# Optimization experiments

Hardware: AMD Instinct MI355X
Metric: run time of the kernel (lower is better)

The kernel has to match this reference:

```python
import jax, jax.numpy as jnp
import numpy as np

B, IC, OC, K, H, W = 8, 512, 512, 3, 32, 32
GAIN, LRMUL = 1.0, 1.0
# compute_runtime_coef: fan_in = prod(weight_shape[:-1])
RC_CONV = GAIN / np.sqrt(K * K * IC) * LRMUL   # conv weight [K,K,IC,OC]
RC_DENSE = GAIN / np.sqrt(IC) * LRMUL          # dense weight [IC, IC]


def setup_inputs() -> dict:
    key = jax.random.key(0)
    ks = jax.random.split(key, 4)
    x = jax.random.normal(ks[0], (B, IC, H, W), dtype=jnp.float32)
    w = jax.random.normal(ks[1], (B, IC), dtype=jnp.float32)
    # init_std = 1/lrmul = 1.0 for both weights; bias init zeros
    conv_w = jax.random.normal(ks[2], (K, K, IC, OC), dtype=jnp.float32)
    dense_w = jax.random.normal(ks[3], (IC, IC), dtype=jnp.float32)
    dense_b = jnp.zeros((IC,), dtype=jnp.float32)
    return {"x": x, "w": w, "conv_w": conv_w, "dense_w": dense_w, "dense_b": dense_b}


def reference(x, w, conv_w, dense_w, dense_b):
    b, ic, h, wd = x.shape
    # modulation: style = Dense(w) + bias + 1
    style = w @ (RC_DENSE * dense_w) + LRMUL * dense_b + 1.0        # [B, IC]
    wt = (RC_CONV * conv_w)[None] * style[:, None, None, :, None]   # [B,K,K,IC,OC]
    # demodulation: rsqrt of sum of squares over (kh, kw, ic)
    d = jax.lax.rsqrt(jnp.sum(jnp.square(wt), axis=(1, 2, 3)) + 1e-8)  # [B, OC]
    wt = wt * d[:, None, None, None, :]
    # grouped conv with groups = batch: weight -> OIHW [B*OC, IC, K, K]
    w_g = jnp.transpose(wt, (0, 4, 3, 1, 2)).reshape(b * OC, ic, K, K)
    xg = x.reshape(1, b * ic, h, wd)
    y = jax.lax.conv_general_dilated(
        xg, w_g, window_strides=(1, 1), padding="SAME",
        dimension_numbers=("NCHW", "OIHW", "NCHW"), feature_group_count=b)
    return y.reshape(b, OC, h, wd)
```

## Files before the change

### kernel.cpp

```cpp
#include <hip/hip_runtime.h>
#include <stdint.h>


#define B_   8
#define IC_  512
#define OC_  512

static constexpr float RC_DENSE = 0.04419417382415922f;
static constexpr float RC_CONV  = 0.014731391274719739f;

typedef _Float16 half8    __attribute__((ext_vector_type(8)));
typedef float    floatx16 __attribute__((ext_vector_type(16)));

__device__ __forceinline__ void g2l(const void* g, void* l) {
  __builtin_amdgcn_global_load_lds(
      (const __attribute__((address_space(1))) void*)g,
      (__attribute__((address_space(3))) void*)l, 16, 0, 0);
}

__global__ __launch_bounds__(256) void style_kernel(
    const float* __restrict__ wv, const float* __restrict__ dw,
    const float* __restrict__ db, float* __restrict__ sm,
    float* __restrict__ sm2) {
  const int b = blockIdx.y;
  const int i = blockIdx.x * 64 + (threadIdx.x & 63);
  const int jg = threadIdx.x >> 6;
  __shared__ float red[4][64];
  float p = 0.f;
  for (int j = jg * 128; j < jg * 128 + 128; ++j)
    p += wv[b * IC_ + j] * dw[(size_t)j * IC_ + i];
  red[jg][threadIdx.x & 63] = p;
  __syncthreads();
  if (threadIdx.x < 64) {
    float s = red[0][threadIdx.x] + red[1][threadIdx.x] +
              red[2][threadIdx.x] + red[3][threadIdx.x];
    s = s * RC_DENSE + db[i] + 1.0f;
    float v = s * RC_CONV;
    sm[b * IC_ + i] = v;
    sm2[b * IC_ + i] = v * v;
  }
}

__global__ __launch_bounds__(256) void prep_kernel(
    const float* __restrict__ cw, const float* __restrict__ x,
    const float* __restrict__ sm, const float* __restrict__ sm2,
    _Float16* __restrict__ Wtf, float* __restrict__ dpart,
    _Float16* __restrict__ xsp) {
  __shared__ __align__(16) char smem[33280];
  const int bid = blockIdx.x;
  const int tid = threadIdx.x;
  if (bid < 256) {
    _Float16* LA = (_Float16*)smem;
    float* redall = (float*)(smem + 18432);
    const int by2 = bid >> 4, icb = bid & 15;
    const int by = by2 >> 1, h2 = by2 & 1;
    const int oc0 = by * 64 + h2 * 32, ic0 = icb * 32;
    const int ocl = tid & 31, g = tid >> 5;
    float sq4[4] = {};
    for (int m = 0; m < 36; ++m) {
      int r = m * 8 + g;
      int t = r >> 5, icl = r & 31;
      float v = cw[(size_t)(t * IC_ + ic0 + icl) * OC_ + oc0 + ocl];
      sq4[m & 3] += v * v;
      LA[m * 256 + ocl * 8 + g] = (_Float16)v;
    }
    for (int b = 0; b < 8; ++b) {
      float p = 0.f;
      for (int s = 0; s < 4; ++s)
        p += sm2[b * IC_ + ic0 + g + 8 * s] * sq4[s];
      redall[(b * 8 + g) * 32 + ocl] = p;
    }
    __syncthreads();
    _Float16* dst = Wtf + (size_t)(by * 16 + icb) * 18432;
    for (int it = 0; it < 5; ++it) {
      int c = it * 256 + tid;
      if (c < 1152) {
        int m = c >> 5, o2 = c & 31;
        *(half8*)(dst + (size_t)(m * 64 + h2 * 32 + o2) * 8) =
            *(const half8*)&LA[m * 256 + o2 * 8];
      }
    }
    const int bb = tid >> 5, o3 = tid & 31;
    float s = 0.f;
    for (int g2 = 0; g2 < 8; ++g2) s += redall[(bb * 8 + g2) * 32 + o3];
    dpart[(size_t)icb * 4096 + bb * OC_ + oc0 + o3] = s;
  } else {
    _Float16* Xt = (_Float16*)smem;
    const int rb = bid - 256;
    const int b = rb >> 5, h = rb & 31;
    for (int k = 0; k < 16; ++k) {
      int idx = k * 256 + tid;
      int ic = idx >> 3, wc = (idx & 7) * 4;
      float4 v = *(const float4*)&x[((size_t)(b * IC_ + ic) * 32 + h) * 32 + wc];
      float s = sm[b * IC_ + ic];
      Xt[(wc + 0) * 520 + ic] = (_Float16)(v.x * s);
      Xt[(wc + 1) * 520 + ic] = (_Float16)(v.y * s);
      Xt[(wc + 2) * 520 + ic] = (_Float16)(v.z * s);
      Xt[(wc + 3) * 520 + ic] = (_Float16)(v.w * s);
    }
    __syncthreads();
    _Float16* xb = xsp + (size_t)b * 16 * 36992;
    const int r = h + 1;
    half8 z = {};
    for (int it = 0; it < 9; ++it) {
      int c = it * 256 + tid;
      if (c < 2176) {
        int icb = c / 136, rem = c - 136 * icb, kkq = rem / 34, C = rem - 34 * kkq;
        half8 val = z;
        if (C != 0 && C != 33)
          val = *(const half8*)&Xt[(C - 1) * 520 + icb * 32 + kkq * 8];
        *(half8*)&xb[(size_t)icb * 36992 + (size_t)r * 1088 + kkq * 272 + C * 8] = val;
      }
    }
    if (h == 0 || h == 31) {
      const int rz = (h == 0) ? 0 : 33;
      for (int it = 0; it < 9; ++it) {
        int c = it * 256 + tid;
        if (c < 2176) {
          int icb = c / 136, rem = c - 136 * icb, kkq = rem / 34, C = rem - 34 * kkq;
          *(half8*)&xb[(size_t)icb * 36992 + (size_t)rz * 1088 + kkq * 272 + C * 8] = z;
        }
      }
    }
  }
}

__global__ __launch_bounds__(256) void conv_kernel(
    const _Float16* __restrict__ Wtf,
    const _Float16* __restrict__ xsp,
    const float* __restrict__ dpart,
    float* __restrict__ out) {
  const int by = blockIdx.x, bx = blockIdx.y, b = blockIdx.z;
  const int tid = threadIdx.x, lane = tid & 63, w = tid >> 6;
  const int wm = w & 1, wn = w >> 1;
  const int n = lane & 31, kq = lane >> 5;
  const int h0 = bx * 4;

  __shared__ _Float16 Xb[2][6528];
  __shared__ float redd[4][64];
  __shared__ float dvl[64];

  const _Float16* gX = xsp + (size_t)b * 16 * 36992 + (size_t)h0 * 1088;
  const _Float16* gA = Wtf + (size_t)(by * 16) * 18432;
  const int aoff = kq * 512 + (wm * 32 + n) * 8;

  for (int i = 0; i < 4; ++i) {
    int c = i * 256 + tid;
    if (c < 816) g2l(gX + (size_t)c * 8, &Xb[0][c * 8]);
  }
  half8 a[9][2], an[9][2];
#pragma unroll
  for (int t = 0; t < 9; ++t)
#pragma unroll
    for (int kk = 0; kk < 2; ++kk)
      a[t][kk] = *(const half8*)(gA + aoff + (t * 2 + kk) * 1024);

  floatx16 acc[2] = {};
  for (int icb = 0; icb < 16; ++icb) {
    const int cur = icb & 1;
    __syncthreads();
    if (icb < 15) {
      const _Float16* gA1 = gA + (size_t)(icb + 1) * 18432 + aoff;
#pragma unroll
      for (int t = 0; t < 9; ++t)
#pragma unroll
        for (int kk = 0; kk < 2; ++kk)
          an[t][kk] = *(const half8*)(gA1 + (t * 2 + kk) * 1024);
      const _Float16* gX1 = gX + (size_t)(icb + 1) * 36992;
      for (int i = 0; i < 4; ++i) {
        int c = i * 256 + tid;
        if (c < 816) g2l(gX1 + (size_t)c * 8, &Xb[cur ^ 1][c * 8]);
      }
    }
    const _Float16* Xp = &Xb[cur][0] + (wn * 2) * 1088 + kq * 272 + n * 8;
#pragma unroll
    for (int s = 0; s < 4; ++s) {
#pragma unroll
      for (int kw = 0; kw < 3; ++kw) {
#pragma unroll
        for (int kk = 0; kk < 2; ++kk) {
          half8 xv = *(const half8*)(Xp + s * 1088 + kk * 544 + kw * 8);
#pragma unroll
          for (int kh = 0; kh < 3; ++kh) {
            int j = s - kh;
            if (j >= 0 && j < 2)
              acc[j] = __builtin_amdgcn_mfma_f32_32x32x16_f16(
                  a[kh * 3 + kw][kk], xv, acc[j], 0, 0, 0);
          }
        }
      }
    }
#pragma unroll
    for (int t = 0; t < 9; ++t) { a[t][0] = an[t][0]; a[t][1] = an[t][1]; }
  }

  __syncthreads();
  {
    const int oc_l = tid & 63, ig = tid >> 6;
    float s = 0.f;
    for (int k = 0; k < 4; ++k)
      s += dpart[(size_t)(ig * 4 + k) * 4096 + b * OC_ + by * 64 + oc_l];
    redd[ig][oc_l] = s;
  }
  __syncthreads();
  if (tid < 64)
    dvl[tid] = rsqrtf(redd[0][tid] + redd[1][tid] + redd[2][tid] +
                      redd[3][tid] + 1e-8f);
  __syncthreads();
  const int oc0 = by * 64 + wm * 32;
  const int r0 = h0 + wn * 2;
#pragma unroll
  for (int rg = 0; rg < 16; ++rg) {
    const int row = (rg & 3) + 8 * (rg >> 2) + 4 * kq;
    const float dv = dvl[wm * 32 + row];
    float* op = out + ((size_t)b * OC_ + oc0 + row) * 1024 + r0 * 32 + n;
    op[0]  = acc[0][rg] * dv;
    op[32] = acc[1][rg] * dv;
  }
}

extern "C" void kernel_launch(void* const* d_in, const int* in_sizes, int n_in,
                              void* d_out, int out_size, void* d_ws, size_t ws_size,
                              hipStream_t stream) {
  const float* x       = (const float*)d_in[0];
  const float* w       = (const float*)d_in[1];
  const float* conv_w  = (const float*)d_in[2];
  const float* dense_w = (const float*)d_in[3];
  const float* dense_b = (const float*)d_in[4];
  float* out = (float*)d_out;

  char* ws = (char*)d_ws;
  float*    sm    = (float*)ws;
  float*    sm2   = (float*)(ws + (16 << 10));
  float*    dpart = (float*)(ws + (32 << 10));
  _Float16* Wtf   = (_Float16*)(ws + (288 << 10));
  _Float16* xsp   = (_Float16*)(ws + (288 << 10) + 4718592);

  style_kernel<<<dim3(8, B_), 256, 0, stream>>>(w, dense_w, dense_b, sm, sm2);
  prep_kernel<<<512, 256, 0, stream>>>(conv_w, x, sm, sm2, Wtf, dpart, xsp);
  conv_kernel<<<dim3(8, 8, B_), 256, 0, stream>>>(Wtf, xsp, dpart, out);
}
```

Before: 130.5 us.

## Stage conv weights through LDS with finer half-block double buffering

The conv kernel now stages weight tiles into LDS with async global-to-LDS loads instead of holding two full sets of per-thread weight registers (current plus prefetch). The pipeline is split into 32 half-k stages, each carrying both an A tile and an X tile, which cuts register pressure, and launch bounds now request 2 blocks per SM for more occupancy. The cost is more barriers, extra LDS reads of the weights, and a larger shared-memory footprint per block.

```diff
diff --git a/kernel.cpp b/kernel.cpp
--- a/kernel.cpp
+++ b/kernel.cpp
@@ -125,7 +125,7 @@
   }
 }
 
-__global__ __launch_bounds__(256) void conv_kernel(
+__global__ __launch_bounds__(256, 2) void conv_kernel(
     const _Float16* __restrict__ Wtf,
     const _Float16* __restrict__ xsp,
     const float* __restrict__ dpart,
@@ -136,62 +136,61 @@
   const int n = lane & 31, kq = lane >> 5;
   const int h0 = bx * 4;
 
-  __shared__ _Float16 Xb[2][6528];
+  __shared__ __align__(16) _Float16 As[2][9216];
+  __shared__ __align__(16) _Float16 Xs[2][3264];
   __shared__ float redd[4][64];
   __shared__ float dvl[64];
 
   const _Float16* gX = xsp + (size_t)b * 16 * 36992 + (size_t)h0 * 1088;
   const _Float16* gA = Wtf + (size_t)(by * 16) * 18432;
-  const int aoff = kq * 512 + (wm * 32 + n) * 8;
-
-  for (int i = 0; i < 4; ++i) {
-    int c = i * 256 + tid;
-    if (c < 816) g2l(gX + (size_t)c * 8, &Xb[0][c * 8]);
-  }
-  half8 a[9][2], an[9][2];
-#pragma unroll
-  for (int t = 0; t < 9; ++t)
-#pragma unroll
-    for (int kk = 0; kk < 2; ++kk)
-      a[t][kk] = *(const half8*)(gA + aoff + (t * 2 + kk) * 1024);
+
+  auto stage = [&](int st, int p) {
+    const int icb = st >> 1, kk = st & 1;
+    const _Float16* a = gA + (size_t)icb * 18432 + kk * 1024;
+#pragma unroll
+    for (int it = 0; it < 5; ++it) {
+      int c = it * 256 + tid;
+      if (c < 1152) {
+        int r = c >> 7, o = c & 127;
+        g2l(a + r * 2048 + o * 8, &As[p][c * 8]);
+      }
+    }
+    const _Float16* xg = gX + (size_t)icb * 36992 + kk * 544;
+#pragma unroll
+    for (int it = 0; it < 2; ++it) {
+      int c = it * 256 + tid;
+      if (c < 408) {
+        int r = c / 68, o = c - r * 68;
+        g2l(xg + r * 1088 + o * 8, &Xs[p][c * 8]);
+      }
+    }
+  };
 
   floatx16 acc[2] = {};
-  for (int icb = 0; icb < 16; ++icb) {
-    const int cur = icb & 1;
+  stage(0, 0);
+  for (int st = 0; st < 32; ++st) {
+    const int cur = st & 1;
     __syncthreads();
-    if (icb < 15) {
-      const _Float16* gA1 = gA + (size_t)(icb + 1) * 18432 + aoff;
-#pragma unroll
-      for (int t = 0; t < 9; ++t)
-#pragma unroll
-        for (int kk = 0; kk < 2; ++kk)
-          an[t][kk] = *(const half8*)(gA1 + (t * 2 + kk) * 1024);
-      const _Float16* gX1 = gX + (size_t)(icb + 1) * 36992;
-      for (int i = 0; i < 4; ++i) {
-        int c = i * 256 + tid;
-        if (c < 816) g2l(gX1 + (size_t)c * 8, &Xb[cur ^ 1][c * 8]);
-      }
-    }
-    const _Float16* Xp = &Xb[cur][0] + (wn * 2) * 1088 + kq * 272 + n * 8;
+    if (st + 1 < 32) stage(st + 1, cur ^ 1);
+    const _Float16* Ap = &As[cur][0] + kq * 512 + (wm * 32 + n) * 8;
+    const _Float16* Xp = &Xs[cur][0] + (wn * 2) * 544 + kq * 272 + n * 8;
+    half8 a[9];
+#pragma unroll
+    for (int t = 0; t < 9; ++t) a[t] = *(const half8*)(Ap + t * 1024);
 #pragma unroll
     for (int s = 0; s < 4; ++s) {
 #pragma unroll
       for (int kw = 0; kw < 3; ++kw) {
-#pragma unroll
-        for (int kk = 0; kk < 2; ++kk) {
-          half8 xv = *(const half8*)(Xp + s * 1088 + kk * 544 + kw * 8);
-#pragma unroll
-          for (int kh = 0; kh < 3; ++kh) {
-            int j = s - kh;
-            if (j >= 0 && j < 2)
-              acc[j] = __builtin_amdgcn_mfma_f32_32x32x16_f16(
-                  a[kh * 3 + kw][kk], xv, acc[j], 0, 0, 0);
-          }
+        half8 xv = *(const half8*)(Xp + s * 544 + kw * 8);
+#pragma unroll
+        for (int kh = 0; kh < 3; ++kh) {
+          int j = s - kh;
+          if (j >= 0 && j < 2)
+            acc[j] = __builtin_amdgcn_mfma_f32_32x32x16_f16(
+                a[kh * 3 + kw], xv, acc[j], 0, 0, 0);
         }
       }
     }
-#pragma unroll
-    for (int t = 0; t < 9; ++t) { a[t][0] = an[t][0]; a[t][1] = an[t][1]; }
   }
 
   __syncthreads();
```

After: 130.2 us. Within noise of the previous version (-0.2%).

## Stage conv weights in LDS and double rows per 512-thread block

Applied to the files above, without the earlier changes.

The conv kernel now uses 512-thread blocks that cover 8 output rows instead of 4, halving the grid to 256 blocks. Each block stages both the weight tile and the input tile into double-buffered dynamic shared memory with async global-to-LDS loads. Previously every wave fetched its own weights from global memory into registers. Hand-placed waitcnt and barriers plus setprio around the MFMA loop aim to overlap the next stage's loads with compute. The cost is about 117 KB of LDS per block, which limits a CU to one block and leaves fewer blocks to hide latency.

```diff
diff --git a/kernel.cpp b/kernel.cpp
--- a/kernel.cpp
+++ b/kernel.cpp
@@ -125,61 +125,83 @@
   }
 }
 
-__global__ __launch_bounds__(256) void conv_kernel(
+__global__ __launch_bounds__(512, 1) void conv_kernel(
     const _Float16* __restrict__ Wtf,
     const _Float16* __restrict__ xsp,
     const float* __restrict__ dpart,
     float* __restrict__ out) {
+  extern __shared__ __align__(16) _Float16 dyn[];
+  _Float16* As0 = dyn;
+  _Float16* As1 = dyn + 18432;
+  _Float16* Xs0 = dyn + 36864;
+  _Float16* Xs1 = dyn + 47744;
+  float* redd = (float*)(dyn + 58624);
+  float* dvl  = redd + 512;
+
   const int by = blockIdx.x, bx = blockIdx.y, b = blockIdx.z;
   const int tid = threadIdx.x, lane = tid & 63, w = tid >> 6;
   const int wm = w & 1, wn = w >> 1;
   const int n = lane & 31, kq = lane >> 5;
-  const int h0 = bx * 4;
-
-  __shared__ _Float16 Xb[2][6528];
-  __shared__ float redd[4][64];
-  __shared__ float dvl[64];
-
+  const int h0 = bx * 8;
+
+  const _Float16* gA = Wtf + (size_t)(by * 16) * 18432;
   const _Float16* gX = xsp + (size_t)b * 16 * 36992 + (size_t)h0 * 1088;
-  const _Float16* gA = Wtf + (size_t)(by * 16) * 18432;
-  const int aoff = kq * 512 + (wm * 32 + n) * 8;
-
-  for (int i = 0; i < 4; ++i) {
-    int c = i * 256 + tid;
-    if (c < 816) g2l(gX + (size_t)c * 8, &Xb[0][c * 8]);
-  }
-  half8 a[9][2], an[9][2];
-#pragma unroll
-  for (int t = 0; t < 9; ++t)
-#pragma unroll
-    for (int kk = 0; kk < 2; ++kk)
-      a[t][kk] = *(const half8*)(gA + aoff + (t * 2 + kk) * 1024);
+
+  auto stage = [&](int icb, int p) {
+    const _Float16* a  = gA + (size_t)icb * 18432;
+    const _Float16* xg = gX + (size_t)icb * 36992;
+    _Float16* Ad = p ? As1 : As0;
+    _Float16* Xd = p ? Xs1 : Xs0;
+#pragma unroll
+    for (int k = 0; k < 4; ++k) {
+      int c = w * 288 + k * 64 + lane;
+      g2l(a + (size_t)c * 8, Ad + c * 8);
+    }
+    {
+      int c = w * 288 + 256 + lane;
+      if (lane < 32) g2l(a + (size_t)c * 8, Ad + c * 8);
+    }
+#pragma unroll
+    for (int k = 0; k < 2; ++k) {
+      int c = w * 170 + k * 64 + lane;
+      g2l(xg + (size_t)c * 8, Xd + c * 8);
+    }
+    {
+      int c = w * 170 + 128 + lane;
+      if (lane < 42) g2l(xg + (size_t)c * 8, Xd + c * 8);
+    }
+  };
 
   floatx16 acc[2] = {};
-  for (int icb = 0; icb < 16; ++icb) {
-    const int cur = icb & 1;
-    __syncthreads();
-    if (icb < 15) {
-      const _Float16* gA1 = gA + (size_t)(icb + 1) * 18432 + aoff;
-#pragma unroll
-      for (int t = 0; t < 9; ++t)
-#pragma unroll
-        for (int kk = 0; kk < 2; ++kk)
-          an[t][kk] = *(const half8*)(gA1 + (t * 2 + kk) * 1024);
-      const _Float16* gX1 = gX + (size_t)(icb + 1) * 36992;
-      for (int i = 0; i < 4; ++i) {
-        int c = i * 256 + tid;
-        if (c < 816) g2l(gX1 + (size_t)c * 8, &Xb[cur ^ 1][c * 8]);
-      }
-    }
-    const _Float16* Xp = &Xb[cur][0] + (wn * 2) * 1088 + kq * 272 + n * 8;
-#pragma unroll
-    for (int s = 0; s < 4; ++s) {
-#pragma unroll
-      for (int kw = 0; kw < 3; ++kw) {
-#pragma unroll
-        for (int kk = 0; kk < 2; ++kk) {
-          half8 xv = *(const half8*)(Xp + s * 1088 + kk * 544 + kw * 8);
+  stage(0, 0);
+  for (int st = 0; st < 16; ++st) {
+    const int cur = st & 1;
+    if (st + 1 < 16) {
+      stage(st + 1, cur ^ 1);
+      __builtin_amdgcn_sched_barrier(0);
+      asm volatile("s_waitcnt vmcnt(8)" ::: "memory");
+    } else {
+      __builtin_amdgcn_sched_barrier(0);
+      asm volatile("s_waitcnt vmcnt(0)" ::: "memory");
+    }
+    __builtin_amdgcn_s_barrier();
+    __builtin_amdgcn_sched_barrier(0);
+    const _Float16* Ar = (cur ? As1 : As0) + kq * 512 + wm * 256 + n * 8;
+    const _Float16* Xr = (cur ? Xs1 : Xs0) + (2 * wn) * 1088 + kq * 272 + n * 8;
+    half8 a[9][2];
+#pragma unroll
+    for (int t = 0; t < 9; ++t) {
+      a[t][0] = *(const half8*)(Ar + (t * 4 + 0) * 512);
+      a[t][1] = *(const half8*)(Ar + (t * 4 + 2) * 512);
+    }
+    __builtin_amdgcn_s_setprio(1);
+#pragma unroll
+    for (int kk = 0; kk < 2; ++kk) {
+#pragma unroll
+      for (int s = 0; s < 4; ++s) {
+#pragma unroll
+        for (int kw = 0; kw < 3; ++kw) {
+          half8 xv = *(const half8*)(Xr + s * 1088 + kk * 544 + kw * 8);
 #pragma unroll
           for (int kh = 0; kh < 3; ++kh) {
             int j = s - kh;
@@ -190,25 +212,28 @@
         }
       }
     }
-#pragma unroll
-    for (int t = 0; t < 9; ++t) { a[t][0] = an[t][0]; a[t][1] = an[t][1]; }
-  }
-
+    __builtin_amdgcn_s_setprio(0);
+    __builtin_amdgcn_sched_barrier(0);
+    __builtin_amdgcn_s_barrier();
+  }
+
+  const int oc0 = by * 64 + wm * 32;
   __syncthreads();
   {
     const int oc_l = tid & 63, ig = tid >> 6;
-    float s = 0.f;
-    for (int k = 0; k < 4; ++k)
-      s += dpart[(size_t)(ig * 4 + k) * 4096 + b * OC_ + by * 64 + oc_l];
-    redd[ig][oc_l] = s;
-  }
-  __syncthreads();
-  if (tid < 64)
-    dvl[tid] = rsqrtf(redd[0][tid] + redd[1][tid] + redd[2][tid] +
-                      redd[3][tid] + 1e-8f);
-  __syncthreads();
-  const int oc0 = by * 64 + wm * 32;
-  const int r0 = h0 + wn * 2;
+    float s = dpart[(size_t)(ig * 2) * 4096 + b * OC_ + by * 64 + oc_l] +
+              dpart[(size_t)(ig * 2 + 1) * 4096 + b * OC_ + by * 64 + oc_l];
+    redd[ig * 64 + oc_l] = s;
+  }
+  __syncthreads();
+  if (tid < 64) {
+    float s = 1e-8f;
+#pragma unroll
+    for (int g = 0; g < 8; ++g) s += redd[g * 64 + tid];
+    dvl[tid] = rsqrtf(s);
+  }
+  __syncthreads();
+  const int r0 = h0 + 2 * wn;
 #pragma unroll
   for (int rg = 0; rg < 16; ++rg) {
     const int row = (rg & 3) + 8 * (rg >> 2) + 4 * kq;
@@ -236,7 +261,14 @@
   _Float16* Wtf   = (_Float16*)(ws + (288 << 10));
   _Float16* xsp   = (_Float16*)(ws + (288 << 10) + 4718592);
 
+  static int dyn_set = 0;
+  if (!dyn_set) {
+    hipFuncSetAttribute((const void*)conv_kernel,
+                        hipFuncAttributeMaxDynamicSharedMemorySize, 119552);
+    dyn_set = 1;
+  }
+
   style_kernel<<<dim3(8, B_), 256, 0, stream>>>(w, dense_w, dense_b, sm, sm2);
   prep_kernel<<<512, 256, 0, stream>>>(conv_w, x, sm, sm2, Wtf, dpart, xsp);
-  conv_kernel<<<dim3(8, 8, B_), 256, 0, stream>>>(Wtf, xsp, dpart, out);
-}
+  conv_kernel<<<dim3(8, 4, B_), 512, 119552, stream>>>(Wtf, xsp, dpart, out);
+}
```

After: 129.3 us. About the same (-0.9%).
